# Performance work log

Hardware: AMD Instinct MI355X
Metric: run time of the kernel (lower is better)

Reference implementation:

```python
import jax, jax.numpy as jnp
import numpy as np

H = 128; N = 64; B = 128; L = 3; F = 7; E = 64; LAT = 128
NEG = -1e9

def _ln(x, g, b, eps=1e-5):
    m = jnp.mean(x, axis=-1, keepdims=True)
    v = jnp.mean((x - m) ** 2, axis=-1, keepdims=True)
    return (x - m) / jnp.sqrt(v + eps) * g + b

def setup_inputs() -> dict:
    key = jax.random.key(0)
    ks = iter(jax.random.split(key, 64))
    def w(shape, s=0.05):
        return (jax.random.normal(next(ks), shape, dtype=jnp.float32) * s)
    inp = {}
    inp['battery_features'] = jax.random.normal(next(ks), (B, F), dtype=jnp.float32)
    inp['material_embeddings'] = jax.random.normal(next(ks), (B, N, E), dtype=jnp.float32)
    inp['node_mask'] = (jax.random.uniform(next(ks), (B, N)) > 0.2).astype(jnp.float32)
    # material encoder: Linear(E,H), LN, ReLU, Linear(H,H), LN, ReLU
    inp['enc_W1'] = w((E, H)); inp['enc_b1'] = jnp.zeros((H,))
    inp['enc_g1'] = jnp.ones((H,)); inp['enc_B1'] = jnp.zeros((H,))
    inp['enc_W2'] = w((H, H)); inp['enc_b2'] = jnp.zeros((H,))
    inp['enc_g2'] = jnp.ones((H,)); inp['enc_B2'] = jnp.zeros((H,))
    # per-layer GATv2 params (stacked over L layers)
    inp['Wq'] = w((L, H, H)); inp['bq'] = jnp.zeros((L, H))
    inp['Wk'] = w((L, H, H)); inp['bk'] = jnp.zeros((L, H))
    inp['Wv'] = w((L, H, H)); inp['bv'] = jnp.zeros((L, H))
    inp['We1'] = w((L, 2 * H, H)); inp['be1'] = jnp.zeros((L, H))
    inp['We2'] = w((L, H)); inp['be2'] = jnp.zeros((L,))
    inp['Wo'] = w((L, H, H)); inp['bo'] = jnp.zeros((L, H))
    inp['o_g'] = jnp.ones((L, H)); inp['o_B'] = jnp.zeros((L, H))
    # legacy decoder: Linear(F+H,H), LN, ReLU, Linear(H,LAT), LN, ReLU, Linear(LAT,F)
    inp['dW1'] = w((F + H, H)); inp['db1'] = jnp.zeros((H,))
    inp['dg1'] = jnp.ones((H,)); inp['dB1'] = jnp.zeros((H,))
    inp['dW2'] = w((H, LAT)); inp['db2'] = jnp.zeros((LAT,))
    inp['dg2'] = jnp.ones((LAT,)); inp['dB2'] = jnp.zeros((LAT,))
    inp['dW3'] = w((LAT, F)); inp['db3'] = jnp.zeros((F,))
    return inp

def reference(battery_features, material_embeddings, node_mask,
              enc_W1, enc_b1, enc_g1, enc_B1, enc_W2, enc_b2, enc_g2, enc_B2,
              Wq, bq, Wk, bk, Wv, bv, We1, be1, We2, be2, Wo, bo, o_g, o_B,
              dW1, db1, dg1, dB1, dW2, db2, dg2, dB2, dW3, db3):
    # material encoder (dropout=0 / eval)
    x = material_embeddings  # [B,N,E]
    h = jax.nn.relu(_ln(x @ enc_W1 + enc_b1, enc_g1, enc_B1))
    h = jax.nn.relu(_ln(h @ enc_W2 + enc_b2, enc_g2, enc_B2))
    x = h * node_mask[..., None]  # [B,N,H]
    mask2d = node_mask[:, :, None] * node_mask[:, None, :]  # [B,N,N]
    nlayers = Wq.shape[0]
    for l in range(nlayers):
        q = x @ Wq[l] + bq[l]
        k = x @ Wk[l] + bk[l]
        v = x @ Wv[l] + bv[l]
        # edge MLP on concat(q_i, k_j): split first linear, avoid concat materialization
        hq = q @ We1[l, :H]          # [B,N,H]
        hk = k @ We1[l, H:]          # [B,N,H]
        eh = jax.nn.relu(hq[:, :, None, :] + hk[:, None, :, :] + be1[l])  # [B,N,N,H]
        scores = jnp.einsum('bijh,h->bij', eh, We2[l]) + be2[l]
        scores = jnp.where(mask2d > 0, scores, NEG)
        attn = jax.nn.softmax(scores, axis=-1) * mask2d
        agg = jnp.einsum('bij,bjh->bih', attn, v)
        x = jax.nn.relu(_ln(agg @ Wo[l] + bo[l], o_g[l], o_B[l]))
        x = x * node_mask[..., None]
    # masked mean pooling
    denom = jnp.clip(jnp.sum(node_mask, axis=1, keepdims=True), 1.0, None)
    pooled = jnp.sum(x * node_mask[..., None], axis=1) / denom  # [B,H]
    d = jnp.concatenate([battery_features, pooled], axis=-1)
    z = jax.nn.relu(_ln(d @ dW1 + db1, dg1, dB1))
    z = jax.nn.relu(_ln(z @ dW2 + db2, dg2, dB2))
    return z @ dW3 + db3  # [B,F] predicted properties
```

## Files before the change

kernel.cpp:

```cpp
#include <hip/hip_runtime.h>


constexpr float EPS = 1e-5f;
constexpr float NEGI = -1e9f;

typedef __bf16 bf16x8 __attribute__((ext_vector_type(8)));
typedef float floatx4 __attribute__((ext_vector_type(4)));

__device__ __forceinline__ bf16x8 cvt8(const float* p) {
  float t[8];
  *(float4*)t = *(const float4*)p;
  *(float4*)(t + 4) = *(const float4*)(p + 4);
  bf16x8 r;
#pragma unroll
  for (int j = 0; j < 8; ++j) r[j] = (__bf16)t[j];
  return r;
}

__global__ __launch_bounds__(256) void prep_kernel(
    const float* __restrict__ Wq, const float* __restrict__ bq,
    const float* __restrict__ Wk, const float* __restrict__ bk,
    const float* __restrict__ bv, const float* __restrict__ We1,
    const float* __restrict__ be1,
    const float* __restrict__ eW1, const float* __restrict__ eW2,
    const float* __restrict__ Wv, const float* __restrict__ Wo,
    __bf16* __restrict__ w1pk, __bf16* __restrict__ w2pk,
    __bf16* __restrict__ wcatpk, __bf16* __restrict__ wopk,
    float* __restrict__ bcat) {
  int tid = threadIdx.x, blk = blockIdx.x;
  if (blk < 48) {
    __shared__ float sB[128 * 16];
    __shared__ float sF[128 * 17];
    int jb = blk >> 3, cc = blk & 7;
    int l = jb >> 1, w = jb & 1;
    const float* A = (w ? Wk : Wq) + l * 16384;
    const float* Bm = We1 + l * 32768 + w * 16384;
    int c0 = cc * 16;
    for (int idx = tid; idx < 2048; idx += 256) {
      int m = idx >> 4, c = idx & 15;
      sB[idx] = Bm[m * 128 + c0 + c];
    }
    __syncthreads();
    int r = tid >> 1, c8 = (tid & 1) * 8;
    float acc[8] = {};
    const float4* A4 = (const float4*)(A + r * 128);
#pragma unroll 8
    for (int k4 = 0; k4 < 32; ++k4) {
      float4 a = A4[k4];
      float av[4] = {a.x, a.y, a.z, a.w};
#pragma unroll
      for (int kk = 0; kk < 4; ++kk)
#pragma unroll
        for (int c = 0; c < 8; ++c)
          acc[c] = fmaf(av[kk], sB[(k4 * 4 + kk) * 16 + c8 + c], acc[c]);
    }
    for (int c = 0; c < 8; ++c) sF[r * 17 + c8 + c] = acc[c];
    __syncthreads();
    int kc = tid >> 6, lane = tid & 63;
    int k0 = kc * 32 + (lane >> 4) * 8, n = lane & 15;
    bf16x8 pk;
#pragma unroll
    for (int j = 0; j < 8; ++j) pk[j] = (__bf16)sF[(k0 + j) * 17 + n];
    int ntg = 8 + w * 8 + cc;
    *((bf16x8*)(wcatpk + l * 49152) + (ntg * 4 + kc) * 64 + lane) = pk;
  } else if (blk < 56) {
    int job = blk - 48;
    const float* src;
    __bf16* dst;
    int KCH = 4;
    if (job == 0) { src = eW1; dst = w1pk; KCH = 2; }
    else if (job == 1) { src = eW2; dst = w2pk; }
    else if (job < 5) { int l = job - 2; src = Wv + l * 16384; dst = wcatpk + l * 49152; }
    else { int l = job - 5; src = Wo + l * 16384; dst = wopk + l * 16384; }
    for (int s = tid; s < 8 * KCH * 64; s += 256) {
      int lane = s & 63, q = s >> 6;
      int kc = q % KCH, nt = q / KCH;
      int k0 = kc * 32 + (lane >> 4) * 8, n = nt * 16 + (lane & 15);
      bf16x8 pk;
#pragma unroll
      for (int j = 0; j < 8; ++j) pk[j] = (__bf16)src[(k0 + j) * 128 + n];
      *((bf16x8*)dst + (nt * KCH + kc) * 64 + lane) = pk;
    }
  } else {
    for (int idx = tid; idx < 3 * 384; idx += 256) {
      int l = idx / 384, c = idx % 384;
      float val;
      if (c < 128) {
        val = bv[l * 128 + c];
      } else if (c < 256) {
        int cc = c - 128;
        float s = 0.f;
        for (int k = 0; k < 128; ++k) s += bq[l * 128 + k] * We1[l * 32768 + k * 128 + cc];
        val = s;
      } else {
        int cc = c - 256;
        float s = be1[l * 128 + cc];
        for (int k = 0; k < 128; ++k) s += bk[l * 128 + k] * We1[l * 32768 + 16384 + k * 128 + cc];
        val = s;
      }
      bcat[l * 384 + c] = val;
    }
  }
}

__global__ __launch_bounds__(256) void enc_qkv_kernel(
    const float* __restrict__ emb, const float* __restrict__ mask,
    const float* __restrict__ eb1, const float* __restrict__ eg1, const float* __restrict__ eB1,
    const float* __restrict__ eb2, const float* __restrict__ eg2, const float* __restrict__ eB2,
    const __bf16* __restrict__ w1pk, const __bf16* __restrict__ w2pk,
    const __bf16* __restrict__ wcat0, const float* __restrict__ bcat0,
    float* __restrict__ hq, float* __restrict__ hk, __bf16* __restrict__ vpk) {
  __shared__ float s_T[32 * 132];
  __shared__ __bf16 s_xpk[32 * 128];
  __shared__ float s_m[32], s_r[32];
  int tid = threadIdx.x, lane = tid & 63, wv = tid >> 6;
  int r0 = blockIdx.x * 32;
  int b = blockIdx.x >> 1, kcv = blockIdx.x & 1;
  int cl = lane & 15, quad = lane >> 4;
  int mt = wv & 1, ntb = (wv >> 1) * 4;

  {
    bf16x8 a1[2];
#pragma unroll
    for (int kc = 0; kc < 2; ++kc)
      a1[kc] = cvt8(emb + (r0 + mt * 16 + cl) * 64 + kc * 32 + quad * 8);
    floatx4 acc[4];
#pragma unroll
    for (int n = 0; n < 4; ++n) acc[n] = 0;
#pragma unroll
    for (int kc = 0; kc < 2; ++kc)
#pragma unroll
      for (int n = 0; n < 4; ++n) {
        bf16x8 bfr = *((const bf16x8*)w1pk + ((ntb + n) * 2 + kc) * 64 + lane);
        acc[n] = __builtin_amdgcn_mfma_f32_16x16x32_bf16(a1[kc], bfr, acc[n], 0, 0, 0);
      }
#pragma unroll
    for (int n = 0; n < 4; ++n) {
      int col = (ntb + n) * 16 + cl;
      float bb = eb1[col];
#pragma unroll
      for (int r = 0; r < 4; ++r) s_T[(mt * 16 + quad * 4 + r) * 132 + col] = acc[n][r] + bb;
    }
  }
  __syncthreads();
  {
    int r = tid >> 3, c0 = tid & 7;
    const float* p = s_T + r * 132 + c0;
    float s = 0.f, q = 0.f;
#pragma unroll
    for (int k = 0; k < 16; ++k) { float v = p[k * 8]; s += v; q += v * v; }
    s += __shfl_xor(s, 1); s += __shfl_xor(s, 2); s += __shfl_xor(s, 4);
    q += __shfl_xor(q, 1); q += __shfl_xor(q, 2); q += __shfl_xor(q, 4);
    if (c0 == 0) {
      float m = s * (1.f / 128.f);
      s_m[r] = m;
      s_r[r] = rsqrtf(fmaxf(q * (1.f / 128.f) - m * m, 0.f) + EPS);
    }
  }
  __syncthreads();
  for (int ch = tid; ch < 512; ch += 256) {
    int r = ch >> 4, c8 = (ch & 15) * 8;
    float vals[8];
    *(float4*)vals = *(const float4*)(s_T + r * 132 + c8);
    *(float4*)(vals + 4) = *(const float4*)(s_T + r * 132 + c8 + 4);
    float m = s_m[r], rs = s_r[r];
    bf16x8 pk;
#pragma unroll
    for (int k = 0; k < 8; ++k)
      pk[k] = (__bf16)fmaxf((vals[k] - m) * rs * eg1[c8 + k] + eB1[c8 + k], 0.f);
    *((bf16x8*)s_xpk + ((r >> 4) * 4 + (c8 >> 5)) * 64 + (((c8 >> 3) & 3) * 16 + (r & 15))) = pk;
  }
  __syncthreads();
  {
    floatx4 acc[4];
#pragma unroll
    for (int n = 0; n < 4; ++n) acc[n] = 0;
    bf16x8 a2[4];
#pragma unroll
    for (int kc = 0; kc < 4; ++kc) a2[kc] = *((const bf16x8*)s_xpk + (mt * 4 + kc) * 64 + lane);
#pragma unroll
    for (int kc = 0; kc < 4; ++kc)
#pragma unroll
      for (int n = 0; n < 4; ++n) {
        bf16x8 bfr = *((const bf16x8*)w2pk + ((ntb + n) * 4 + kc) * 64 + lane);
        acc[n] = __builtin_amdgcn_mfma_f32_16x16x32_bf16(a2[kc], bfr, acc[n], 0, 0, 0);
      }
    __syncthreads();
#pragma unroll
    for (int n = 0; n < 4; ++n) {
      int col = (ntb + n) * 16 + cl;
      float bb = eb2[col];
#pragma unroll
      for (int r = 0; r < 4; ++r) s_T[(mt * 16 + quad * 4 + r) * 132 + col] = acc[n][r] + bb;
    }
  }
  __syncthreads();
  {
    int r = tid >> 3, c0 = tid & 7;
    const float* p = s_T + r * 132 + c0;
    float s = 0.f, q = 0.f;
#pragma unroll
    for (int k = 0; k < 16; ++k) { float v = p[k * 8]; s += v; q += v * v; }
    s += __shfl_xor(s, 1); s += __shfl_xor(s, 2); s += __shfl_xor(s, 4);
    q += __shfl_xor(q, 1); q += __shfl_xor(q, 2); q += __shfl_xor(q, 4);
    if (c0 == 0) {
      float m = s * (1.f / 128.f);
      s_m[r] = m;
      s_r[r] = rsqrtf(fmaxf(q * (1.f / 128.f) - m * m, 0.f) + EPS);
    }
  }
  __syncthreads();
  for (int ch = tid; ch < 512; ch += 256) {
    int r = ch >> 4, c8 = (ch & 15) * 8;
    float vals[8];
    *(float4*)vals = *(const float4*)(s_T + r * 132 + c8);
    *(float4*)(vals + 4) = *(const float4*)(s_T + r * 132 + c8 + 4);
    float m = s_m[r], rs = s_r[r], mk = mask[r0 + r];
    bf16x8 pk;
#pragma unroll
    for (int k = 0; k < 8; ++k)
      pk[k] = (__bf16)(fmaxf((vals[k] - m) * rs * eg2[c8 + k] + eB2[c8 + k], 0.f) * mk);
    *((bf16x8*)s_xpk + ((r >> 4) * 4 + (c8 >> 5)) * 64 + (((c8 >> 3) & 3) * 16 + (r & 15))) = pk;
  }
  __syncthreads();
  {
    int ntq = (wv >> 1) * 12;
    bf16x8 aq[4];
#pragma unroll
    for (int kc = 0; kc < 4; ++kc) aq[kc] = *((const bf16x8*)s_xpk + (mt * 4 + kc) * 64 + lane);
    floatx4 acc[12];
#pragma unroll
    for (int n = 0; n < 12; ++n) acc[n] = 0;
#pragma unroll
    for (int kc = 0; kc < 4; ++kc)
#pragma unroll
      for (int n = 0; n < 12; ++n) {
        bf16x8 bfr = *((const bf16x8*)wcat0 + ((ntq + n) * 4 + kc) * 64 + lane);
        acc[n] = __builtin_amdgcn_mfma_f32_16x16x32_bf16(aq[kc], bfr, acc[n], 0, 0, 0);
      }
#pragma unroll
    for (int n = 0; n < 12; ++n) {
      int nt = ntq + n;
      if (nt < 8) {
        int col = nt * 16 + cl;
        float bb = bcat0[col];
#pragma unroll
        for (int r = 0; r < 4; ++r) s_T[(mt * 16 + quad * 4 + r) * 132 + col] = acc[n][r] + bb;
      } else if (nt < 16) {
        int col = (nt - 8) * 16 + cl;
        float bb = bcat0[128 + col];
#pragma unroll
        for (int r = 0; r < 4; ++r) hq[(r0 + mt * 16 + quad * 4 + r) * 128 + col] = acc[n][r] + bb;
      } else {
        int col = (nt - 16) * 16 + cl;
        float bb = bcat0[256 + col];
#pragma unroll
        for (int r = 0; r < 4; ++r) hk[(r0 + mt * 16 + quad * 4 + r) * 128 + col] = acc[n][r] + bb;
      }
    }
  }
  __syncthreads();
  for (int s = tid; s < 512; s += 256) {
    int lane2 = s & 63, nt = s >> 6;
    int q2 = lane2 >> 4, c2 = lane2 & 15;
    bf16x8 pk;
#pragma unroll
    for (int jj = 0; jj < 8; ++jj) pk[jj] = (__bf16)s_T[(q2 * 8 + jj) * 132 + nt * 16 + c2];
    ((bf16x8*)(vpk + b * 8192))[(nt * 2 + kcv) * 64 + lane2] = pk;
  }
}

template <bool LAST>
__global__ __launch_bounds__(256) void layer_kernel(
    const float* __restrict__ hq_in, const float* __restrict__ hk_in,
    const __bf16* __restrict__ vpk_in, const float* __restrict__ mask,
    const float* __restrict__ We2, const float* __restrict__ be2p,
    const __bf16* __restrict__ wopk_l, const float* __restrict__ bo_l,
    const float* __restrict__ og_l, const float* __restrict__ oB_l,
    const __bf16* __restrict__ wcat_n, const float* __restrict__ bcat_n,
    float* __restrict__ hq_out, float* __restrict__ hk_out,
    __bf16* __restrict__ vpk_out, float* __restrict__ xout) {
  __shared__ float s_hk[64 * 132];
  __shared__ float s_hq[16 * 132];
  __shared__ float s_at[16 * 68];
  __shared__ float s_agg[16 * 132];
  __shared__ float s_T[16 * 132];
  __shared__ __bf16 s_xpk[16 * 128];
  __shared__ float s_m[16], s_r[16];
  __shared__ float s_mk[64];
  int tid = threadIdx.x, lane = tid & 63, wv = tid >> 6;
  int b = blockIdx.x >> 2, i0 = (blockIdx.x & 3) * 16;
  int cl = lane & 15, quad = lane >> 4;

  {
    const float4* src = (const float4*)(hk_in + b * 8192);
    for (int idx = tid; idx < 2048; idx += 256) {
      int row = idx >> 5, c4 = (idx & 31) * 4;
      *(float4*)(s_hk + row * 132 + c4) = src[idx];
    }
    const float4* srq = (const float4*)(hq_in + (b * 64 + i0) * 128);
    for (int idx = tid; idx < 512; idx += 256) {
      int row = idx >> 5, c4 = (idx & 31) * 4;
      *(float4*)(s_hq + row * 132 + c4) = srq[idx];
    }
    if (tid < 64) s_mk[tid] = mask[b * 64 + tid];
  }
  __syncthreads();

  {
    int j = lane;
    float mj = s_mk[j];
    float accs[4] = {};
#pragma unroll
    for (int half = 0; half < 2; ++half) {
      float4 hkv[16], w2v[16];
#pragma unroll
      for (int q = 0; q < 16; ++q) hkv[q] = *(const float4*)(s_hk + j * 132 + half * 64 + q * 4);
#pragma unroll
      for (int q = 0; q < 16; ++q) w2v[q] = *(const float4*)(We2 + half * 64 + q * 4);
#pragma unroll
      for (int kk = 0; kk < 4; ++kk) {
        int il = wv * 4 + kk;
        const float4* hq4 = (const float4*)(s_hq + il * 132 + half * 64);
        float a0 = 0.f, a1 = 0.f, a2 = 0.f, a3 = 0.f;
#pragma unroll
        for (int q = 0; q < 16; ++q) {
          float4 h4 = hq4[q], k4 = hkv[q], w4 = w2v[q];
          a0 = fmaf(fmaxf(h4.x + k4.x, 0.f), w4.x, a0);
          a1 = fmaf(fmaxf(h4.y + k4.y, 0.f), w4.y, a1);
          a2 = fmaf(fmaxf(h4.z + k4.z, 0.f), w4.z, a2);
          a3 = fmaf(fmaxf(h4.w + k4.w, 0.f), w4.w, a3);
        }
        accs[kk] += (a0 + a1) + (a2 + a3);
      }
    }
    float be2v = be2p[0];
#pragma unroll
    for (int kk = 0; kk < 4; ++kk) {
      int il = wv * 4 + kk;
      float m2 = s_mk[i0 + il] * mj;
      float sc = (m2 > 0.f) ? accs[kk] + be2v : NEGI;
      float mx = sc;
#pragma unroll
      for (int off = 32; off >= 1; off >>= 1) mx = fmaxf(mx, __shfl_xor(mx, off));
      float p = __expf(sc - mx);
      float sm = p;
#pragma unroll
      for (int off = 32; off >= 1; off >>= 1) sm += __shfl_xor(sm, off);
      s_at[il * 68 + j] = p / sm * m2;
    }
  }
  __syncthreads();

  {
    bf16x8 aat[2];
#pragma unroll
    for (int kc = 0; kc < 2; ++kc) aat[kc] = cvt8(s_at + cl * 68 + kc * 32 + quad * 8);
    const bf16x8* vb = (const bf16x8*)(vpk_in + b * 8192);
    floatx4 acc[2];
    acc[0] = 0; acc[1] = 0;
#pragma unroll
    for (int kc = 0; kc < 2; ++kc)
#pragma unroll
      for (int n = 0; n < 2; ++n) {
        bf16x8 bfr = vb[((2 * wv + n) * 2 + kc) * 64 + lane];
        acc[n] = __builtin_amdgcn_mfma_f32_16x16x32_bf16(aat[kc], bfr, acc[n], 0, 0, 0);
      }
#pragma unroll
    for (int n = 0; n < 2; ++n) {
      int col = (2 * wv + n) * 16 + cl;
#pragma unroll
      for (int r = 0; r < 4; ++r) s_agg[(quad * 4 + r) * 132 + col] = acc[n][r];
    }
  }
  __syncthreads();

  {
    bf16x8 ag[4];
#pragma unroll
    for (int kc = 0; kc < 4; ++kc) ag[kc] = cvt8(s_agg + cl * 132 + kc * 32 + quad * 8);
    floatx4 acc[2];
    acc[0] = 0; acc[1] = 0;
#pragma unroll
    for (int kc = 0; kc < 4; ++kc)
#pragma unroll
      for (int n = 0; n < 2; ++n) {
        bf16x8 bfr = *((const bf16x8*)wopk_l + ((2 * wv + n) * 4 + kc) * 64 + lane);
        acc[n] = __builtin_amdgcn_mfma_f32_16x16x32_bf16(ag[kc], bfr, acc[n], 0, 0, 0);
      }
#pragma unroll
    for (int n = 0; n < 2; ++n) {
      int col = (2 * wv + n) * 16 + cl;
      float bb = bo_l[col];
#pragma unroll
      for (int r = 0; r < 4; ++r) s_T[(quad * 4 + r) * 132 + col] = acc[n][r] + bb;
    }
  }
  __syncthreads();

  {
    int r = tid >> 4, c0 = tid & 15;
    const float* p = s_T + r * 132 + c0;
    float s = 0.f, q = 0.f;
#pragma unroll
    for (int k = 0; k < 8; ++k) { float v = p[k * 16]; s += v; q += v * v; }
    s += __shfl_xor(s, 1); s += __shfl_xor(s, 2); s += __shfl_xor(s, 4); s += __shfl_xor(s, 8);
    q += __shfl_xor(q, 1); q += __shfl_xor(q, 2); q += __shfl_xor(q, 4); q += __shfl_xor(q, 8);
    if (c0 == 0) {
      float m = s * (1.f / 128.f);
      s_m[r] = m;
      s_r[r] = rsqrtf(fmaxf(q * (1.f / 128.f) - m * m, 0.f) + EPS);
    }
  }
  __syncthreads();
  {
    int r = tid >> 4, c8 = (tid & 15) * 8;
    float vals[8];
    *(float4*)vals = *(const float4*)(s_T + r * 132 + c8);
    *(float4*)(vals + 4) = *(const float4*)(s_T + r * 132 + c8 + 4);
    float m = s_m[r], rs = s_r[r], mk = s_mk[i0 + r];
#pragma unroll
    for (int k = 0; k < 8; ++k)
      vals[k] = fmaxf((vals[k] - m) * rs * og_l[c8 + k] + oB_l[c8 + k], 0.f) * mk;
    if (LAST) {
      float* xp = xout + (b * 64 + i0 + r) * 128 + c8;
      *(float4*)xp = *(float4*)vals;
      *(float4*)(xp + 4) = *(float4*)(vals + 4);
    } else {
      bf16x8 pk;
#pragma unroll
      for (int k = 0; k < 8; ++k) pk[k] = (__bf16)vals[k];
      *((bf16x8*)s_xpk + (c8 >> 5) * 64 + (((c8 >> 3) & 3) * 16 + r)) = pk;
    }
  }
  if (!LAST) {
    __syncthreads();
    {
      bf16x8 ax[4];
#pragma unroll
      for (int kc = 0; kc < 4; ++kc) ax[kc] = *((const bf16x8*)s_xpk + kc * 64 + lane);
      floatx4 acc[6];
#pragma unroll
      for (int n = 0; n < 6; ++n) acc[n] = 0;
#pragma unroll
      for (int kc = 0; kc < 4; ++kc)
#pragma unroll
        for (int n = 0; n < 6; ++n) {
          bf16x8 bfr = *((const bf16x8*)wcat_n + ((wv * 6 + n) * 4 + kc) * 64 + lane);
          acc[n] = __builtin_amdgcn_mfma_f32_16x16x32_bf16(ax[kc], bfr, acc[n], 0, 0, 0);
        }
#pragma unroll
      for (int n = 0; n < 6; ++n) {
        int nt = wv * 6 + n;
        if (nt < 8) {
          int col = nt * 16 + cl;
          float bb = bcat_n[col];
#pragma unroll
          for (int r = 0; r < 4; ++r) s_T[(quad * 4 + r) * 132 + col] = acc[n][r] + bb;
        } else if (nt < 16) {
          int col = (nt - 8) * 16 + cl;
          float bb = bcat_n[128 + col];
#pragma unroll
          for (int r = 0; r < 4; ++r) hq_out[(b * 64 + i0 + quad * 4 + r) * 128 + col] = acc[n][r] + bb;
        } else {
          int col = (nt - 16) * 16 + cl;
          float bb = bcat_n[256 + col];
#pragma unroll
          for (int r = 0; r < 4; ++r) hk_out[(b * 64 + i0 + quad * 4 + r) * 128 + col] = acc[n][r] + bb;
        }
      }
    }
    __syncthreads();
    {
      int kcv = i0 >> 5, q0 = (i0 & 31) >> 3;
      int nt = tid >> 5, dq = (tid >> 4) & 1, c2 = tid & 15;
      int qg = q0 + dq;
      bf16x8 pk;
#pragma unroll
      for (int jj = 0; jj < 8; ++jj) pk[jj] = (__bf16)s_T[(dq * 8 + jj) * 132 + nt * 16 + c2];
      ((bf16x8*)(vpk_out + b * 8192))[(nt * 2 + kcv) * 64 + qg * 16 + c2] = pk;
    }
  }
}

__device__ __forceinline__ float ln128(float val, float g, float be, int t, float* red) {
  float s = val, q = val * val;
#pragma unroll
  for (int off = 32; off >= 1; off >>= 1) {
    s += __shfl_xor(s, off);
    q += __shfl_xor(q, off);
  }
  if ((t & 63) == 0) { red[(t >> 6) * 2] = s; red[(t >> 6) * 2 + 1] = q; }
  __syncthreads();
  float S = red[0] + red[2], Q = red[1] + red[3];
  __syncthreads();
  float m = S * (1.f / 128.f);
  float var = Q * (1.f / 128.f) - m * m;
  float r = rsqrtf(fmaxf(var, 0.f) + EPS);
  return (val - m) * r * g + be;
}

__global__ __launch_bounds__(128) void dec_kernel(
    const float* __restrict__ bf, const float* __restrict__ x, const float* __restrict__ mask,
    const float* __restrict__ dW1, const float* __restrict__ db1,
    const float* __restrict__ dg1, const float* __restrict__ dB1,
    const float* __restrict__ dW2, const float* __restrict__ db2,
    const float* __restrict__ dg2, const float* __restrict__ dB2,
    const float* __restrict__ dW3, const float* __restrict__ db3,
    float* __restrict__ out) {
  __shared__ float s_d[136];
  __shared__ float s_z[128];
  __shared__ float red[4];
  __shared__ float s_mk[64];
  int b = blockIdx.x, t = threadIdx.x;
  if (t < 64) s_mk[t] = mask[b * 64 + t];
  __syncthreads();
  float den = 0.f;
#pragma unroll
  for (int i = 0; i < 64; ++i) den += s_mk[i];
  den = fmaxf(den, 1.f);
  float pooled = 0.f;
  const float* xb = x + b * 8192;
  for (int i = 0; i < 64; ++i) pooled += xb[i * 128 + t];
  pooled /= den;
  if (t < 7) s_d[t] = bf[b * 7 + t];
  s_d[7 + t] = pooled;
  __syncthreads();

  float z = db1[t];
  for (int k = 0; k < 135; ++k) z = fmaf(s_d[k], dW1[k * 128 + t], z);
  z = ln128(z, dg1[t], dB1[t], t, red);
  z = fmaxf(z, 0.f);
  s_z[t] = z;
  __syncthreads();

  float z2 = db2[t];
  for (int k = 0; k < 128; ++k) z2 = fmaf(s_z[k], dW2[k * 128 + t], z2);
  z2 = ln128(z2, dg2[t], dB2[t], t, red);
  z2 = fmaxf(z2, 0.f);
  s_z[t] = z2;
  __syncthreads();

  if (t < 7) {
    float o = db3[t];
    for (int k = 0; k < 128; ++k) o = fmaf(s_z[k], dW3[k * 7 + t], o);
    out[b * 7 + t] = o;
  }
}

extern "C" void kernel_launch(void* const* d_in, const int* in_sizes, int n_in,
                              void* d_out, int out_size, void* d_ws, size_t ws_size,
                              hipStream_t stream) {
  const float* bf   = (const float*)d_in[0];
  const float* emb  = (const float*)d_in[1];
  const float* mask = (const float*)d_in[2];
  const float* eW1 = (const float*)d_in[3];
  const float* eb1 = (const float*)d_in[4];
  const float* eg1 = (const float*)d_in[5];
  const float* eB1 = (const float*)d_in[6];
  const float* eW2 = (const float*)d_in[7];
  const float* eb2 = (const float*)d_in[8];
  const float* eg2 = (const float*)d_in[9];
  const float* eB2 = (const float*)d_in[10];
  const float* Wq = (const float*)d_in[11];
  const float* bq = (const float*)d_in[12];
  const float* Wk = (const float*)d_in[13];
  const float* bk = (const float*)d_in[14];
  const float* Wv = (const float*)d_in[15];
  const float* bv = (const float*)d_in[16];
  const float* We1 = (const float*)d_in[17];
  const float* be1 = (const float*)d_in[18];
  const float* We2 = (const float*)d_in[19];
  const float* be2 = (const float*)d_in[20];
  const float* Wo = (const float*)d_in[21];
  const float* bo = (const float*)d_in[22];
  const float* og = (const float*)d_in[23];
  const float* oB = (const float*)d_in[24];
  const float* dW1 = (const float*)d_in[25];
  const float* db1 = (const float*)d_in[26];
  const float* dg1 = (const float*)d_in[27];
  const float* dB1 = (const float*)d_in[28];
  const float* dW2 = (const float*)d_in[29];
  const float* db2 = (const float*)d_in[30];
  const float* dg2 = (const float*)d_in[31];
  const float* dB2 = (const float*)d_in[32];
  const float* dW3 = (const float*)d_in[33];
  const float* db3 = (const float*)d_in[34];
  float* out = (float*)d_out;

  float* ws = (float*)d_ws;
  float* hqA  = ws;
  float* hkA  = ws + 1048576;
  float* hqB  = ws + 2 * 1048576;
  float* hkB  = ws + 3 * 1048576;
  float* x    = ws + 4 * 1048576;
  float* bcat = ws + 5 * 1048576;
  __bf16* bb16  = (__bf16*)(ws + 5 * 1048576 + 2048);
  __bf16* vpkA  = bb16;
  __bf16* vpkB  = bb16 + 1048576;
  __bf16* wcatpk = bb16 + 2 * 1048576;
  __bf16* wopk   = wcatpk + 3 * 49152;
  __bf16* w1pk   = wopk + 3 * 16384;
  __bf16* w2pk   = w1pk + 8192;

  prep_kernel<<<57, 256, 0, stream>>>(Wq, bq, Wk, bk, bv, We1, be1,
                                      eW1, eW2, Wv, Wo, w1pk, w2pk, wcatpk, wopk, bcat);
  enc_qkv_kernel<<<256, 256, 0, stream>>>(emb, mask, eb1, eg1, eB1, eb2, eg2, eB2,
                                          w1pk, w2pk, wcatpk, bcat, hqA, hkA, vpkA);
  layer_kernel<false><<<512, 256, 0, stream>>>(
      hqA, hkA, vpkA, mask, We2, be2, wopk, bo, og, oB,
      wcatpk + 49152, bcat + 384, hqB, hkB, vpkB, nullptr);
  layer_kernel<false><<<512, 256, 0, stream>>>(
      hqB, hkB, vpkB, mask, We2 + 128, be2 + 1, wopk + 16384, bo + 128, og + 128, oB + 128,
      wcatpk + 2 * 49152, bcat + 2 * 384, hqA, hkA, vpkA, nullptr);
  layer_kernel<true><<<512, 256, 0, stream>>>(
      hqA, hkA, vpkA, mask, We2 + 256, be2 + 2, wopk + 2 * 16384, bo + 256, og + 256, oB + 256,
      nullptr, nullptr, nullptr, nullptr, nullptr, x);
  dec_kernel<<<128, 128, 0, stream>>>(bf, x, mask, dW1, db1, dg1, dB1,
                                      dW2, db2, dg2, dB2, dW3, db3, out);
}
```

Baseline: 223.4 us.

## Fuse encoder, all GAT layers and decoder into one per-batch mega kernel

Replaces the encoder, three per-layer kernels and the decoder with a single 512-thread kernel, one block per batch element, that keeps activations, hq/hk and V in shared memory across layers. The edge-score loop now works in packed fp16 pairs with dot2 accumulation, pooling is folded into the last LayerNorm, and the decoder matvecs are split over four thread groups. This removes global round trips and launch gaps between stages. In exchange only 128 blocks run, which leaves much of the GPU idle, and the fp16 edge scores reduce precision.

```diff
diff --git a/kernel.cpp b/kernel.cpp
--- a/kernel.cpp
+++ b/kernel.cpp
@@ -6,6 +6,9 @@
 
 typedef __bf16 bf16x8 __attribute__((ext_vector_type(8)));
 typedef float floatx4 __attribute__((ext_vector_type(4)));
+typedef _Float16 h2 __attribute__((ext_vector_type(2)));
+
+union U32H2 { unsigned int u; h2 h; };
 
 __device__ __forceinline__ bf16x8 cvt8(const float* p) {
   float t[8];
@@ -15,6 +18,14 @@
 #pragma unroll
   for (int j = 0; j < 8; ++j) r[j] = (__bf16)t[j];
   return r;
+}
+
+__device__ __forceinline__ float fdot2h(h2 a, h2 b, float c) {
+#if __has_builtin(__builtin_amdgcn_fdot2)
+  return __builtin_amdgcn_fdot2(a, b, c, false);
+#else
+  return c + (float)a[0] * (float)b[0] + (float)a[1] * (float)b[1];
+#endif
 }
 
 __global__ __launch_bounds__(256) void prep_kernel(
@@ -103,448 +114,404 @@
   }
 }
 
-__global__ __launch_bounds__(256) void enc_qkv_kernel(
+__device__ __forceinline__ void ln512(unsigned char* SM, const float* __restrict__ g,
+                                      const float* __restrict__ be, float mreg,
+                                      bool domask, bool dopack, bool dopool, int tid) {
+  float* SF = (float*)(SM + 16384);
+  int r = tid >> 3, c0 = tid & 7;
+  const float* base = SF + r * 128;
+  float s = 0.f, q = 0.f;
+#pragma unroll
+  for (int k = 0; k < 16; ++k) {
+    float v = base[(c0 + 8 * k + 4 * r) & 127];
+    s += v; q += v * v;
+  }
+  s += __shfl_xor(s, 1); s += __shfl_xor(s, 2); s += __shfl_xor(s, 4);
+  q += __shfl_xor(q, 1); q += __shfl_xor(q, 2); q += __shfl_xor(q, 4);
+  float m = s * (1.f / 128.f);
+  float rs = rsqrtf(fmaxf(q * (1.f / 128.f) - m * m, 0.f) + EPS);
+  float mk = domask ? __shfl(mreg, r) : 1.f;
+  int c8 = c0 * 16;
+  float vals[16];
+#pragma unroll
+  for (int tq = 0; tq < 4; ++tq)
+    *(float4*)(vals + tq * 4) = *(const float4*)(base + ((c8 + 4 * r + 4 * tq) & 127));
+#pragma unroll
+  for (int k2 = 0; k2 < 16; ++k2) {
+    int c = c8 + k2;
+    vals[k2] = fmaxf((vals[k2] - m) * rs * g[c] + be[c], 0.f) * mk;
+  }
+  if (dopack) {
+#pragma unroll
+    for (int hh = 0; hh < 2; ++hh) {
+      int ch = c8 + hh * 8;
+      bf16x8 pk;
+#pragma unroll
+      for (int j2 = 0; j2 < 8; ++j2) pk[j2] = (__bf16)vals[hh * 8 + j2];
+      ((bf16x8*)SM)[((r >> 4) * 4 + (ch >> 5)) * 64 + ((ch >> 3) & 3) * 16 + (r & 15)] = pk;
+    }
+  }
+  if (dopool) {
+    float* SP = (float*)(SM + 49152);
+#pragma unroll
+    for (int k2 = 0; k2 < 16; ++k2) {
+      float v = vals[k2];
+      v += __shfl_xor(v, 8); v += __shfl_xor(v, 16); v += __shfl_xor(v, 32);
+      vals[k2] = v;
+    }
+    int lane = tid & 63, wvv = tid >> 6;
+    if ((lane >> 3) == 0) {
+#pragma unroll
+      for (int tq = 0; tq < 4; ++tq)
+        *(float4*)(SP + wvv * 128 + c8 + tq * 4) = *(float4*)(vals + tq * 4);
+    }
+  }
+}
+
+__global__ __launch_bounds__(512, 2) void mega_kernel(
     const float* __restrict__ emb, const float* __restrict__ mask,
+    const float* __restrict__ bfeat,
     const float* __restrict__ eb1, const float* __restrict__ eg1, const float* __restrict__ eB1,
     const float* __restrict__ eb2, const float* __restrict__ eg2, const float* __restrict__ eB2,
     const __bf16* __restrict__ w1pk, const __bf16* __restrict__ w2pk,
-    const __bf16* __restrict__ wcat0, const float* __restrict__ bcat0,
-    float* __restrict__ hq, float* __restrict__ hk, __bf16* __restrict__ vpk) {
-  __shared__ float s_T[32 * 132];
-  __shared__ __bf16 s_xpk[32 * 128];
-  __shared__ float s_m[32], s_r[32];
-  int tid = threadIdx.x, lane = tid & 63, wv = tid >> 6;
-  int r0 = blockIdx.x * 32;
-  int b = blockIdx.x >> 1, kcv = blockIdx.x & 1;
-  int cl = lane & 15, quad = lane >> 4;
-  int mt = wv & 1, ntb = (wv >> 1) * 4;
-
-  {
-    bf16x8 a1[2];
-#pragma unroll
-    for (int kc = 0; kc < 2; ++kc)
-      a1[kc] = cvt8(emb + (r0 + mt * 16 + cl) * 64 + kc * 32 + quad * 8);
-    floatx4 acc[4];
-#pragma unroll
-    for (int n = 0; n < 4; ++n) acc[n] = 0;
-#pragma unroll
-    for (int kc = 0; kc < 2; ++kc)
-#pragma unroll
-      for (int n = 0; n < 4; ++n) {
-        bf16x8 bfr = *((const bf16x8*)w1pk + ((ntb + n) * 2 + kc) * 64 + lane);
-        acc[n] = __builtin_amdgcn_mfma_f32_16x16x32_bf16(a1[kc], bfr, acc[n], 0, 0, 0);
-      }
-#pragma unroll
-    for (int n = 0; n < 4; ++n) {
-      int col = (ntb + n) * 16 + cl;
-      float bb = eb1[col];
-#pragma unroll
-      for (int r = 0; r < 4; ++r) s_T[(mt * 16 + quad * 4 + r) * 132 + col] = acc[n][r] + bb;
-    }
-  }
-  __syncthreads();
-  {
-    int r = tid >> 3, c0 = tid & 7;
-    const float* p = s_T + r * 132 + c0;
-    float s = 0.f, q = 0.f;
-#pragma unroll
-    for (int k = 0; k < 16; ++k) { float v = p[k * 8]; s += v; q += v * v; }
-    s += __shfl_xor(s, 1); s += __shfl_xor(s, 2); s += __shfl_xor(s, 4);
-    q += __shfl_xor(q, 1); q += __shfl_xor(q, 2); q += __shfl_xor(q, 4);
-    if (c0 == 0) {
-      float m = s * (1.f / 128.f);
-      s_m[r] = m;
-      s_r[r] = rsqrtf(fmaxf(q * (1.f / 128.f) - m * m, 0.f) + EPS);
-    }
-  }
-  __syncthreads();
-  for (int ch = tid; ch < 512; ch += 256) {
-    int r = ch >> 4, c8 = (ch & 15) * 8;
-    float vals[8];
-    *(float4*)vals = *(const float4*)(s_T + r * 132 + c8);
-    *(float4*)(vals + 4) = *(const float4*)(s_T + r * 132 + c8 + 4);
-    float m = s_m[r], rs = s_r[r];
-    bf16x8 pk;
-#pragma unroll
-    for (int k = 0; k < 8; ++k)
-      pk[k] = (__bf16)fmaxf((vals[k] - m) * rs * eg1[c8 + k] + eB1[c8 + k], 0.f);
-    *((bf16x8*)s_xpk + ((r >> 4) * 4 + (c8 >> 5)) * 64 + (((c8 >> 3) & 3) * 16 + (r & 15))) = pk;
-  }
-  __syncthreads();
-  {
-    floatx4 acc[4];
-#pragma unroll
-    for (int n = 0; n < 4; ++n) acc[n] = 0;
-    bf16x8 a2[4];
-#pragma unroll
-    for (int kc = 0; kc < 4; ++kc) a2[kc] = *((const bf16x8*)s_xpk + (mt * 4 + kc) * 64 + lane);
-#pragma unroll
-    for (int kc = 0; kc < 4; ++kc)
-#pragma unroll
-      for (int n = 0; n < 4; ++n) {
-        bf16x8 bfr = *((const bf16x8*)w2pk + ((ntb + n) * 4 + kc) * 64 + lane);
-        acc[n] = __builtin_amdgcn_mfma_f32_16x16x32_bf16(a2[kc], bfr, acc[n], 0, 0, 0);
-      }
-    __syncthreads();
-#pragma unroll
-    for (int n = 0; n < 4; ++n) {
-      int col = (ntb + n) * 16 + cl;
-      float bb = eb2[col];
-#pragma unroll
-      for (int r = 0; r < 4; ++r) s_T[(mt * 16 + quad * 4 + r) * 132 + col] = acc[n][r] + bb;
-    }
-  }
-  __syncthreads();
-  {
-    int r = tid >> 3, c0 = tid & 7;
-    const float* p = s_T + r * 132 + c0;
-    float s = 0.f, q = 0.f;
-#pragma unroll
-    for (int k = 0; k < 16; ++k) { float v = p[k * 8]; s += v; q += v * v; }
-    s += __shfl_xor(s, 1); s += __shfl_xor(s, 2); s += __shfl_xor(s, 4);
-    q += __shfl_xor(q, 1); q += __shfl_xor(q, 2); q += __shfl_xor(q, 4);
-    if (c0 == 0) {
-      float m = s * (1.f / 128.f);
-      s_m[r] = m;
-      s_r[r] = rsqrtf(fmaxf(q * (1.f / 128.f) - m * m, 0.f) + EPS);
-    }
-  }
-  __syncthreads();
-  for (int ch = tid; ch < 512; ch += 256) {
-    int r = ch >> 4, c8 = (ch & 15) * 8;
-    float vals[8];
-    *(float4*)vals = *(const float4*)(s_T + r * 132 + c8);
-    *(float4*)(vals + 4) = *(const float4*)(s_T + r * 132 + c8 + 4);
-    float m = s_m[r], rs = s_r[r], mk = mask[r0 + r];
-    bf16x8 pk;
-#pragma unroll
-    for (int k = 0; k < 8; ++k)
-      pk[k] = (__bf16)(fmaxf((vals[k] - m) * rs * eg2[c8 + k] + eB2[c8 + k], 0.f) * mk);
-    *((bf16x8*)s_xpk + ((r >> 4) * 4 + (c8 >> 5)) * 64 + (((c8 >> 3) & 3) * 16 + (r & 15))) = pk;
-  }
-  __syncthreads();
-  {
-    int ntq = (wv >> 1) * 12;
-    bf16x8 aq[4];
-#pragma unroll
-    for (int kc = 0; kc < 4; ++kc) aq[kc] = *((const bf16x8*)s_xpk + (mt * 4 + kc) * 64 + lane);
-    floatx4 acc[12];
-#pragma unroll
-    for (int n = 0; n < 12; ++n) acc[n] = 0;
-#pragma unroll
-    for (int kc = 0; kc < 4; ++kc)
-#pragma unroll
-      for (int n = 0; n < 12; ++n) {
-        bf16x8 bfr = *((const bf16x8*)wcat0 + ((ntq + n) * 4 + kc) * 64 + lane);
-        acc[n] = __builtin_amdgcn_mfma_f32_16x16x32_bf16(aq[kc], bfr, acc[n], 0, 0, 0);
-      }
-#pragma unroll
-    for (int n = 0; n < 12; ++n) {
-      int nt = ntq + n;
-      if (nt < 8) {
-        int col = nt * 16 + cl;
-        float bb = bcat0[col];
-#pragma unroll
-        for (int r = 0; r < 4; ++r) s_T[(mt * 16 + quad * 4 + r) * 132 + col] = acc[n][r] + bb;
-      } else if (nt < 16) {
-        int col = (nt - 8) * 16 + cl;
-        float bb = bcat0[128 + col];
-#pragma unroll
-        for (int r = 0; r < 4; ++r) hq[(r0 + mt * 16 + quad * 4 + r) * 128 + col] = acc[n][r] + bb;
-      } else {
-        int col = (nt - 16) * 16 + cl;
-        float bb = bcat0[256 + col];
-#pragma unroll
-        for (int r = 0; r < 4; ++r) hk[(r0 + mt * 16 + quad * 4 + r) * 128 + col] = acc[n][r] + bb;
-      }
-    }
-  }
-  __syncthreads();
-  for (int s = tid; s < 512; s += 256) {
-    int lane2 = s & 63, nt = s >> 6;
-    int q2 = lane2 >> 4, c2 = lane2 & 15;
-    bf16x8 pk;
-#pragma unroll
-    for (int jj = 0; jj < 8; ++jj) pk[jj] = (__bf16)s_T[(q2 * 8 + jj) * 132 + nt * 16 + c2];
-    ((bf16x8*)(vpk + b * 8192))[(nt * 2 + kcv) * 64 + lane2] = pk;
-  }
-}
-
-template <bool LAST>
-__global__ __launch_bounds__(256) void layer_kernel(
-    const float* __restrict__ hq_in, const float* __restrict__ hk_in,
-    const __bf16* __restrict__ vpk_in, const float* __restrict__ mask,
-    const float* __restrict__ We2, const float* __restrict__ be2p,
-    const __bf16* __restrict__ wopk_l, const float* __restrict__ bo_l,
-    const float* __restrict__ og_l, const float* __restrict__ oB_l,
-    const __bf16* __restrict__ wcat_n, const float* __restrict__ bcat_n,
-    float* __restrict__ hq_out, float* __restrict__ hk_out,
-    __bf16* __restrict__ vpk_out, float* __restrict__ xout) {
-  __shared__ float s_hk[64 * 132];
-  __shared__ float s_hq[16 * 132];
-  __shared__ float s_at[16 * 68];
-  __shared__ float s_agg[16 * 132];
-  __shared__ float s_T[16 * 132];
-  __shared__ __bf16 s_xpk[16 * 128];
-  __shared__ float s_m[16], s_r[16];
-  __shared__ float s_mk[64];
-  int tid = threadIdx.x, lane = tid & 63, wv = tid >> 6;
-  int b = blockIdx.x >> 2, i0 = (blockIdx.x & 3) * 16;
-  int cl = lane & 15, quad = lane >> 4;
-
-  {
-    const float4* src = (const float4*)(hk_in + b * 8192);
-    for (int idx = tid; idx < 2048; idx += 256) {
-      int row = idx >> 5, c4 = (idx & 31) * 4;
-      *(float4*)(s_hk + row * 132 + c4) = src[idx];
-    }
-    const float4* srq = (const float4*)(hq_in + (b * 64 + i0) * 128);
-    for (int idx = tid; idx < 512; idx += 256) {
-      int row = idx >> 5, c4 = (idx & 31) * 4;
-      *(float4*)(s_hq + row * 132 + c4) = srq[idx];
-    }
-    if (tid < 64) s_mk[tid] = mask[b * 64 + tid];
-  }
-  __syncthreads();
-
-  {
-    int j = lane;
-    float mj = s_mk[j];
-    float accs[4] = {};
-#pragma unroll
-    for (int half = 0; half < 2; ++half) {
-      float4 hkv[16], w2v[16];
-#pragma unroll
-      for (int q = 0; q < 16; ++q) hkv[q] = *(const float4*)(s_hk + j * 132 + half * 64 + q * 4);
-#pragma unroll
-      for (int q = 0; q < 16; ++q) w2v[q] = *(const float4*)(We2 + half * 64 + q * 4);
-#pragma unroll
-      for (int kk = 0; kk < 4; ++kk) {
-        int il = wv * 4 + kk;
-        const float4* hq4 = (const float4*)(s_hq + il * 132 + half * 64);
-        float a0 = 0.f, a1 = 0.f, a2 = 0.f, a3 = 0.f;
-#pragma unroll
-        for (int q = 0; q < 16; ++q) {
-          float4 h4 = hq4[q], k4 = hkv[q], w4 = w2v[q];
-          a0 = fmaf(fmaxf(h4.x + k4.x, 0.f), w4.x, a0);
-          a1 = fmaf(fmaxf(h4.y + k4.y, 0.f), w4.y, a1);
-          a2 = fmaf(fmaxf(h4.z + k4.z, 0.f), w4.z, a2);
-          a3 = fmaf(fmaxf(h4.w + k4.w, 0.f), w4.w, a3);
-        }
-        accs[kk] += (a0 + a1) + (a2 + a3);
-      }
-    }
-    float be2v = be2p[0];
-#pragma unroll
-    for (int kk = 0; kk < 4; ++kk) {
-      int il = wv * 4 + kk;
-      float m2 = s_mk[i0 + il] * mj;
-      float sc = (m2 > 0.f) ? accs[kk] + be2v : NEGI;
-      float mx = sc;
-#pragma unroll
-      for (int off = 32; off >= 1; off >>= 1) mx = fmaxf(mx, __shfl_xor(mx, off));
-      float p = __expf(sc - mx);
-      float sm = p;
-#pragma unroll
-      for (int off = 32; off >= 1; off >>= 1) sm += __shfl_xor(sm, off);
-      s_at[il * 68 + j] = p / sm * m2;
-    }
-  }
-  __syncthreads();
-
-  {
-    bf16x8 aat[2];
-#pragma unroll
-    for (int kc = 0; kc < 2; ++kc) aat[kc] = cvt8(s_at + cl * 68 + kc * 32 + quad * 8);
-    const bf16x8* vb = (const bf16x8*)(vpk_in + b * 8192);
-    floatx4 acc[2];
-    acc[0] = 0; acc[1] = 0;
-#pragma unroll
-    for (int kc = 0; kc < 2; ++kc)
-#pragma unroll
-      for (int n = 0; n < 2; ++n) {
-        bf16x8 bfr = vb[((2 * wv + n) * 2 + kc) * 64 + lane];
-        acc[n] = __builtin_amdgcn_mfma_f32_16x16x32_bf16(aat[kc], bfr, acc[n], 0, 0, 0);
-      }
-#pragma unroll
-    for (int n = 0; n < 2; ++n) {
-      int col = (2 * wv + n) * 16 + cl;
-#pragma unroll
-      for (int r = 0; r < 4; ++r) s_agg[(quad * 4 + r) * 132 + col] = acc[n][r];
-    }
-  }
-  __syncthreads();
-
-  {
-    bf16x8 ag[4];
-#pragma unroll
-    for (int kc = 0; kc < 4; ++kc) ag[kc] = cvt8(s_agg + cl * 132 + kc * 32 + quad * 8);
-    floatx4 acc[2];
-    acc[0] = 0; acc[1] = 0;
-#pragma unroll
-    for (int kc = 0; kc < 4; ++kc)
-#pragma unroll
-      for (int n = 0; n < 2; ++n) {
-        bf16x8 bfr = *((const bf16x8*)wopk_l + ((2 * wv + n) * 4 + kc) * 64 + lane);
-        acc[n] = __builtin_amdgcn_mfma_f32_16x16x32_bf16(ag[kc], bfr, acc[n], 0, 0, 0);
-      }
-#pragma unroll
-    for (int n = 0; n < 2; ++n) {
-      int col = (2 * wv + n) * 16 + cl;
-      float bb = bo_l[col];
-#pragma unroll
-      for (int r = 0; r < 4; ++r) s_T[(quad * 4 + r) * 132 + col] = acc[n][r] + bb;
-    }
-  }
-  __syncthreads();
-
-  {
-    int r = tid >> 4, c0 = tid & 15;
-    const float* p = s_T + r * 132 + c0;
-    float s = 0.f, q = 0.f;
-#pragma unroll
-    for (int k = 0; k < 8; ++k) { float v = p[k * 16]; s += v; q += v * v; }
-    s += __shfl_xor(s, 1); s += __shfl_xor(s, 2); s += __shfl_xor(s, 4); s += __shfl_xor(s, 8);
-    q += __shfl_xor(q, 1); q += __shfl_xor(q, 2); q += __shfl_xor(q, 4); q += __shfl_xor(q, 8);
-    if (c0 == 0) {
-      float m = s * (1.f / 128.f);
-      s_m[r] = m;
-      s_r[r] = rsqrtf(fmaxf(q * (1.f / 128.f) - m * m, 0.f) + EPS);
-    }
-  }
-  __syncthreads();
-  {
-    int r = tid >> 4, c8 = (tid & 15) * 8;
-    float vals[8];
-    *(float4*)vals = *(const float4*)(s_T + r * 132 + c8);
-    *(float4*)(vals + 4) = *(const float4*)(s_T + r * 132 + c8 + 4);
-    float m = s_m[r], rs = s_r[r], mk = s_mk[i0 + r];
-#pragma unroll
-    for (int k = 0; k < 8; ++k)
-      vals[k] = fmaxf((vals[k] - m) * rs * og_l[c8 + k] + oB_l[c8 + k], 0.f) * mk;
-    if (LAST) {
-      float* xp = xout + (b * 64 + i0 + r) * 128 + c8;
-      *(float4*)xp = *(float4*)vals;
-      *(float4*)(xp + 4) = *(float4*)(vals + 4);
-    } else {
-      bf16x8 pk;
-#pragma unroll
-      for (int k = 0; k < 8; ++k) pk[k] = (__bf16)vals[k];
-      *((bf16x8*)s_xpk + (c8 >> 5) * 64 + (((c8 >> 3) & 3) * 16 + r)) = pk;
-    }
-  }
-  if (!LAST) {
-    __syncthreads();
-    {
-      bf16x8 ax[4];
-#pragma unroll
-      for (int kc = 0; kc < 4; ++kc) ax[kc] = *((const bf16x8*)s_xpk + kc * 64 + lane);
-      floatx4 acc[6];
-#pragma unroll
-      for (int n = 0; n < 6; ++n) acc[n] = 0;
-#pragma unroll
-      for (int kc = 0; kc < 4; ++kc)
-#pragma unroll
-        for (int n = 0; n < 6; ++n) {
-          bf16x8 bfr = *((const bf16x8*)wcat_n + ((wv * 6 + n) * 4 + kc) * 64 + lane);
-          acc[n] = __builtin_amdgcn_mfma_f32_16x16x32_bf16(ax[kc], bfr, acc[n], 0, 0, 0);
-        }
-#pragma unroll
-      for (int n = 0; n < 6; ++n) {
-        int nt = wv * 6 + n;
-        if (nt < 8) {
-          int col = nt * 16 + cl;
-          float bb = bcat_n[col];
-#pragma unroll
-          for (int r = 0; r < 4; ++r) s_T[(quad * 4 + r) * 132 + col] = acc[n][r] + bb;
-        } else if (nt < 16) {
-          int col = (nt - 8) * 16 + cl;
-          float bb = bcat_n[128 + col];
-#pragma unroll
-          for (int r = 0; r < 4; ++r) hq_out[(b * 64 + i0 + quad * 4 + r) * 128 + col] = acc[n][r] + bb;
-        } else {
-          int col = (nt - 16) * 16 + cl;
-          float bb = bcat_n[256 + col];
-#pragma unroll
-          for (int r = 0; r < 4; ++r) hk_out[(b * 64 + i0 + quad * 4 + r) * 128 + col] = acc[n][r] + bb;
-        }
-      }
-    }
-    __syncthreads();
-    {
-      int kcv = i0 >> 5, q0 = (i0 & 31) >> 3;
-      int nt = tid >> 5, dq = (tid >> 4) & 1, c2 = tid & 15;
-      int qg = q0 + dq;
-      bf16x8 pk;
-#pragma unroll
-      for (int jj = 0; jj < 8; ++jj) pk[jj] = (__bf16)s_T[(dq * 8 + jj) * 132 + nt * 16 + c2];
-      ((bf16x8*)(vpk_out + b * 8192))[(nt * 2 + kcv) * 64 + qg * 16 + c2] = pk;
-    }
-  }
-}
-
-__device__ __forceinline__ float ln128(float val, float g, float be, int t, float* red) {
-  float s = val, q = val * val;
-#pragma unroll
-  for (int off = 32; off >= 1; off >>= 1) {
-    s += __shfl_xor(s, off);
-    q += __shfl_xor(q, off);
-  }
-  if ((t & 63) == 0) { red[(t >> 6) * 2] = s; red[(t >> 6) * 2 + 1] = q; }
-  __syncthreads();
-  float S = red[0] + red[2], Q = red[1] + red[3];
-  __syncthreads();
-  float m = S * (1.f / 128.f);
-  float var = Q * (1.f / 128.f) - m * m;
-  float r = rsqrtf(fmaxf(var, 0.f) + EPS);
-  return (val - m) * r * g + be;
-}
-
-__global__ __launch_bounds__(128) void dec_kernel(
-    const float* __restrict__ bf, const float* __restrict__ x, const float* __restrict__ mask,
+    const __bf16* __restrict__ wcatpk, const float* __restrict__ bcat,
+    const float* __restrict__ We2, const float* __restrict__ be2,
+    const __bf16* __restrict__ wopk, const float* __restrict__ bo,
+    const float* __restrict__ og, const float* __restrict__ oB,
     const float* __restrict__ dW1, const float* __restrict__ db1,
     const float* __restrict__ dg1, const float* __restrict__ dB1,
     const float* __restrict__ dW2, const float* __restrict__ db2,
     const float* __restrict__ dg2, const float* __restrict__ dB2,
     const float* __restrict__ dW3, const float* __restrict__ db3,
     float* __restrict__ out) {
-  __shared__ float s_d[136];
-  __shared__ float s_z[128];
-  __shared__ float red[4];
-  __shared__ float s_mk[64];
-  int b = blockIdx.x, t = threadIdx.x;
-  if (t < 64) s_mk[t] = mask[b * 64 + t];
-  __syncthreads();
-  float den = 0.f;
-#pragma unroll
-  for (int i = 0; i < 64; ++i) den += s_mk[i];
+  __shared__ __align__(16) unsigned char SM[65536];
+  __bf16* SX = (__bf16*)SM;
+  unsigned int* LQ = (unsigned int*)(SM + 16384);
+  unsigned int* LK = (unsigned int*)(SM + 32768);
+  float* SF = (float*)(SM + 16384);
+  __bf16* SV = (__bf16*)(SM + 49152);
+  float* SP = (float*)(SM + 49152);
+  float* sd  = (float*)(SM + 53248);
+  float* sz  = (float*)(SM + 53824);
+  float* sz2 = (float*)(SM + 54336);
+  float* red = (float*)(SM + 54848);
+
+  int tid = threadIdx.x;
+  int lane = tid & 63, wv = tid >> 6;
+  int quad = lane >> 4, cl = lane & 15;
+  int b = blockIdx.x;
+  const float* embb = emb + b * 4096;
+  float mreg = mask[b * 64 + lane];
+
+  {
+    bf16x8 a[4][2];
+#pragma unroll
+    for (int mt = 0; mt < 4; ++mt)
+#pragma unroll
+      for (int kc = 0; kc < 2; ++kc)
+        a[mt][kc] = cvt8(embb + (mt * 16 + cl) * 64 + kc * 32 + quad * 8);
+    floatx4 acc[4];
+#pragma unroll
+    for (int mt = 0; mt < 4; ++mt) acc[mt] = 0;
+#pragma unroll
+    for (int kc = 0; kc < 2; ++kc) {
+      bf16x8 bw = *((const bf16x8*)w1pk + (wv * 2 + kc) * 64 + lane);
+#pragma unroll
+      for (int mt = 0; mt < 4; ++mt)
+        acc[mt] = __builtin_amdgcn_mfma_f32_16x16x32_bf16(a[mt][kc], bw, acc[mt], 0, 0, 0);
+    }
+    int col = wv * 16 + cl;
+    float bb = eb1[col];
+#pragma unroll
+    for (int mt = 0; mt < 4; ++mt)
+#pragma unroll
+      for (int r = 0; r < 4; ++r) {
+        int row = mt * 16 + quad * 4 + r;
+        SF[row * 128 + ((col + 4 * row) & 127)] = acc[mt][r] + bb;
+      }
+  }
+  __syncthreads();
+  ln512(SM, eg1, eB1, mreg, false, true, false, tid);
+  __syncthreads();
+
+  {
+    bf16x8 a[4][4];
+#pragma unroll
+    for (int mt = 0; mt < 4; ++mt)
+#pragma unroll
+      for (int kc = 0; kc < 4; ++kc)
+        a[mt][kc] = *((const bf16x8*)SX + (mt * 4 + kc) * 64 + lane);
+    floatx4 acc[4];
+#pragma unroll
+    for (int mt = 0; mt < 4; ++mt) acc[mt] = 0;
+#pragma unroll
+    for (int kc = 0; kc < 4; ++kc) {
+      bf16x8 bw = *((const bf16x8*)w2pk + (wv * 4 + kc) * 64 + lane);
+#pragma unroll
+      for (int mt = 0; mt < 4; ++mt)
+        acc[mt] = __builtin_amdgcn_mfma_f32_16x16x32_bf16(a[mt][kc], bw, acc[mt], 0, 0, 0);
+    }
+    __syncthreads();
+    int col = wv * 16 + cl;
+    float bb = eb2[col];
+#pragma unroll
+    for (int mt = 0; mt < 4; ++mt)
+#pragma unroll
+      for (int r = 0; r < 4; ++r) {
+        int row = mt * 16 + quad * 4 + r;
+        SF[row * 128 + ((col + 4 * row) & 127)] = acc[mt][r] + bb;
+      }
+  }
+  __syncthreads();
+  ln512(SM, eg2, eB2, mreg, true, true, false, tid);
+  __syncthreads();
+
+  for (int l = 0; l < 3; ++l) {
+    const bf16x8* wc = (const bf16x8*)(wcatpk + l * 49152);
+    const bf16x8* wo = (const bf16x8*)(wopk + l * 16384);
+    const float* bc = bcat + l * 384;
+    const float* we2l = We2 + l * 128;
+    float be2v = be2[l];
+    const float* bol = bo + l * 128;
+    const float* ogl = og + l * 128;
+    const float* oBl = oB + l * 128;
+
+    {
+      bf16x8 a[4][4];
+#pragma unroll
+      for (int mt = 0; mt < 4; ++mt)
+#pragma unroll
+        for (int kc = 0; kc < 4; ++kc)
+          a[mt][kc] = *((const bf16x8*)SX + (mt * 4 + kc) * 64 + lane);
+      floatx4 acc[3][4];
+#pragma unroll
+      for (int n = 0; n < 3; ++n)
+#pragma unroll
+        for (int mt = 0; mt < 4; ++mt) acc[n][mt] = 0;
+#pragma unroll
+      for (int kc = 0; kc < 4; ++kc)
+#pragma unroll
+        for (int n = 0; n < 3; ++n) {
+          bf16x8 bw = wc[((wv * 3 + n) * 4 + kc) * 64 + lane];
+#pragma unroll
+          for (int mt = 0; mt < 4; ++mt)
+            acc[n][mt] = __builtin_amdgcn_mfma_f32_16x16x32_bf16(a[mt][kc], bw, acc[n][mt], 0, 0, 0);
+        }
+#pragma unroll
+      for (int n = 0; n < 3; ++n) {
+        int g = wv * 3 + n;
+        if (g < 8) {
+          float bb = bc[g * 16 + cl];
+#pragma unroll
+          for (int mt = 0; mt < 4; ++mt)
+#pragma unroll
+            for (int r = 0; r < 4; ++r) {
+              int j = mt * 16 + quad * 4 + r;
+              SV[((g * 2 + (j >> 5)) * 64 + ((j >> 3) & 3) * 16 + cl) * 8 + (j & 7)] =
+                  (__bf16)(acc[n][mt][r] + bb);
+            }
+        } else if (g < 16) {
+          int h = (g - 8) * 16 + cl;
+          float bb = bc[128 + h];
+          int hp = h >> 1;
+#pragma unroll
+          for (int mt = 0; mt < 4; ++mt)
+#pragma unroll
+            for (int r = 0; r < 4; ++r) {
+              int i = mt * 16 + quad * 4 + r;
+              *(_Float16*)(SM + 16384 + (hp * 64 + ((i + hp) & 63)) * 4 + (h & 1) * 2) =
+                  (_Float16)(acc[n][mt][r] + bb);
+            }
+        } else {
+          int h = (g - 16) * 16 + cl;
+          float bb = bc[256 + h];
+          int hp = h >> 1;
+#pragma unroll
+          for (int mt = 0; mt < 4; ++mt)
+#pragma unroll
+            for (int r = 0; r < 4; ++r) {
+              int j = mt * 16 + quad * 4 + r;
+              *(_Float16*)(SM + 32768 + (hp * 64 + ((j + hp) & 63)) * 4 + (h & 1) * 2) =
+                  (_Float16)(acc[n][mt][r] + bb);
+            }
+        }
+      }
+    }
+    __syncthreads();
+
+    {
+      int i0 = wv * 8;
+      unsigned int hq_u[8];
+#pragma unroll
+      for (int ii = 0; ii < 8; ++ii)
+        hq_u[ii] = LQ[lane * 64 + ((i0 + ii + lane) & 63)];
+      U32H2 w2c;
+      w2c.h[0] = (_Float16)we2l[2 * lane];
+      w2c.h[1] = (_Float16)we2l[2 * lane + 1];
+      float acc8[8];
+#pragma unroll
+      for (int ii = 0; ii < 8; ++ii) acc8[ii] = 0.f;
+      h2 hz = {(_Float16)0.0f, (_Float16)0.0f};
+#pragma unroll
+      for (int hp = 0; hp < 64; ++hp) {
+        U32H2 hk; hk.u = LK[hp * 64 + ((lane + hp) & 63)];
+        U32H2 w2h; w2h.u = (unsigned int)__shfl((int)w2c.u, hp);
+#pragma unroll
+        for (int ii = 0; ii < 8; ++ii) {
+          U32H2 hq; hq.u = (unsigned int)__shfl((int)hq_u[ii], hp);
+          h2 s2 = hq.h + hk.h;
+          s2 = __builtin_elementwise_max(s2, hz);
+          acc8[ii] = fdot2h(s2, w2h.h, acc8[ii]);
+        }
+      }
+      float mj = mreg;
+#pragma unroll
+      for (int ii = 0; ii < 8; ++ii) {
+        int i = i0 + ii;
+        float mi = __shfl(mreg, i);
+        float m2 = mi * mj;
+        float sc = (m2 > 0.f) ? acc8[ii] + be2v : NEGI;
+        float mx = sc;
+#pragma unroll
+        for (int off = 32; off >= 1; off >>= 1) mx = fmaxf(mx, __shfl_xor(mx, off));
+        float p = __expf(sc - mx);
+        float sm = p;
+#pragma unroll
+        for (int off = 32; off >= 1; off >>= 1) sm += __shfl_xor(sm, off);
+        ((__bf16*)SM)[i * 72 + lane] = (__bf16)(p / sm * m2);
+      }
+    }
+    __syncthreads();
+
+    {
+      bf16x8 aat[4][2];
+#pragma unroll
+      for (int mt = 0; mt < 4; ++mt)
+#pragma unroll
+        for (int kc = 0; kc < 2; ++kc)
+          aat[mt][kc] = *(const bf16x8*)(SM + ((mt * 16 + cl) * 72 + kc * 32 + quad * 8) * 2);
+      __syncthreads();
+      floatx4 acc[4];
+#pragma unroll
+      for (int mt = 0; mt < 4; ++mt) acc[mt] = 0;
+#pragma unroll
+      for (int kc = 0; kc < 2; ++kc) {
+        bf16x8 bw = ((const bf16x8*)SV)[(wv * 2 + kc) * 64 + lane];
+#pragma unroll
+        for (int mt = 0; mt < 4; ++mt)
+          acc[mt] = __builtin_amdgcn_mfma_f32_16x16x32_bf16(aat[mt][kc], bw, acc[mt], 0, 0, 0);
+      }
+      int hcol = wv * 16 + cl;
+      int kc2 = hcol >> 5, q2 = (hcol >> 3) & 3, jj = hcol & 7;
+#pragma unroll
+      for (int mt = 0; mt < 4; ++mt)
+#pragma unroll
+        for (int r = 0; r < 4; ++r) {
+          int i = mt * 16 + quad * 4 + r;
+          SX[((mt * 4 + kc2) * 64 + q2 * 16 + (i & 15)) * 8 + jj] = (__bf16)acc[mt][r];
+        }
+    }
+    __syncthreads();
+
+    {
+      bf16x8 a[4][4];
+#pragma unroll
+      for (int mt = 0; mt < 4; ++mt)
+#pragma unroll
+        for (int kc = 0; kc < 4; ++kc)
+          a[mt][kc] = *((const bf16x8*)SX + (mt * 4 + kc) * 64 + lane);
+      floatx4 acc[4];
+#pragma unroll
+      for (int mt = 0; mt < 4; ++mt) acc[mt] = 0;
+#pragma unroll
+      for (int kc = 0; kc < 4; ++kc) {
+        bf16x8 bw = wo[(wv * 4 + kc) * 64 + lane];
+#pragma unroll
+        for (int mt = 0; mt < 4; ++mt)
+          acc[mt] = __builtin_amdgcn_mfma_f32_16x16x32_bf16(a[mt][kc], bw, acc[mt], 0, 0, 0);
+      }
+      int col = wv * 16 + cl;
+      float bb = bol[col];
+#pragma unroll
+      for (int mt = 0; mt < 4; ++mt)
+#pragma unroll
+        for (int r = 0; r < 4; ++r) {
+          int row = mt * 16 + quad * 4 + r;
+          SF[row * 128 + ((col + 4 * row) & 127)] = acc[mt][r] + bb;
+        }
+    }
+    __syncthreads();
+    ln512(SM, ogl, oBl, mreg, true, l < 2, l == 2, tid);
+    __syncthreads();
+  }
+
+  float den = mreg;
+#pragma unroll
+  for (int off = 32; off >= 1; off >>= 1) den += __shfl_xor(den, off);
   den = fmaxf(den, 1.f);
-  float pooled = 0.f;
-  const float* xb = x + b * 8192;
-  for (int i = 0; i < 64; ++i) pooled += xb[i * 128 + t];
-  pooled /= den;
-  if (t < 7) s_d[t] = bf[b * 7 + t];
-  s_d[7 + t] = pooled;
-  __syncthreads();
-
-  float z = db1[t];
-  for (int k = 0; k < 135; ++k) z = fmaf(s_d[k], dW1[k * 128 + t], z);
-  z = ln128(z, dg1[t], dB1[t], t, red);
-  z = fmaxf(z, 0.f);
-  s_z[t] = z;
-  __syncthreads();
-
-  float z2 = db2[t];
-  for (int k = 0; k < 128; ++k) z2 = fmaf(s_z[k], dW2[k * 128 + t], z2);
-  z2 = ln128(z2, dg2[t], dB2[t], t, red);
-  z2 = fmaxf(z2, 0.f);
-  s_z[t] = z2;
-  __syncthreads();
-
-  if (t < 7) {
-    float o = db3[t];
-    for (int k = 0; k < 128; ++k) o = fmaf(s_z[k], dW3[k * 7 + t], o);
-    out[b * 7 + t] = o;
+
+  if (tid < 7) sd[tid] = bfeat[b * 7 + tid];
+  if (tid < 128) {
+    float s = 0.f;
+#pragma unroll
+    for (int w = 0; w < 8; ++w) s += SP[w * 128 + tid];
+    sd[7 + tid] = s / den;
+  }
+  __syncthreads();
+
+  int t = tid & 127, g4 = tid >> 7;
+  {
+    float zp = 0.f;
+    for (int k = g4; k < 135; k += 4) zp = fmaf(sd[k], dW1[k * 128 + t], zp);
+    SP[g4 * 128 + t] = zp;
+  }
+  __syncthreads();
+  float z = db1[t] + SP[t] + SP[128 + t] + SP[256 + t] + SP[384 + t];
+  {
+    float s = z, q = z * z;
+#pragma unroll
+    for (int off = 32; off >= 1; off >>= 1) { s += __shfl_xor(s, off); q += __shfl_xor(q, off); }
+    if (lane == 0) { red[wv] = s; red[8 + wv] = q; }
+    __syncthreads();
+    float S = 0.f, Q = 0.f;
+#pragma unroll
+    for (int w = 0; w < 8; ++w) { S += red[w]; Q += red[8 + w]; }
+    S *= 0.25f; Q *= 0.25f;
+    float m = S * (1.f / 128.f);
+    float rs = rsqrtf(fmaxf(Q * (1.f / 128.f) - m * m, 0.f) + EPS);
+    z = fmaxf((z - m) * rs * dg1[t] + dB1[t], 0.f);
+    __syncthreads();
+  }
+  sz[t] = z;
+  __syncthreads();
+  {
+    float zp = 0.f;
+    for (int k = g4; k < 128; k += 4) zp = fmaf(sz[k], dW2[k * 128 + t], zp);
+    SP[g4 * 128 + t] = zp;
+  }
+  __syncthreads();
+  float z2 = db2[t] + SP[t] + SP[128 + t] + SP[256 + t] + SP[384 + t];
+  {
+    float s = z2, q = z2 * z2;
+#pragma unroll
+    for (int off = 32; off >= 1; off >>= 1) { s += __shfl_xor(s, off); q += __shfl_xor(q, off); }
+    if (lane == 0) { red[wv] = s; red[8 + wv] = q; }
+    __syncthreads();
+    float S = 0.f, Q = 0.f;
+#pragma unroll
+    for (int w = 0; w < 8; ++w) { S += red[w]; Q += red[8 + w]; }
+    S *= 0.25f; Q *= 0.25f;
+    float m = S * (1.f / 128.f);
+    float rs = rsqrtf(fmaxf(Q * (1.f / 128.f) - m * m, 0.f) + EPS);
+    z2 = fmaxf((z2 - m) * rs * dg2[t] + dB2[t], 0.f);
+    __syncthreads();
+  }
+  sz2[t] = z2;
+  __syncthreads();
+  if (tid < 7) {
+    float o = db3[tid];
+    for (int k = 0; k < 128; ++k) o = fmaf(sz2[k], dW3[k * 7 + tid], o);
+    out[b * 7 + tid] = o;
   }
 }
 
@@ -589,33 +556,16 @@
   float* out = (float*)d_out;
 
   float* ws = (float*)d_ws;
-  float* hqA  = ws;
-  float* hkA  = ws + 1048576;
-  float* hqB  = ws + 2 * 1048576;
-  float* hkB  = ws + 3 * 1048576;
-  float* x    = ws + 4 * 1048576;
-  float* bcat = ws + 5 * 1048576;
-  __bf16* bb16  = (__bf16*)(ws + 5 * 1048576 + 2048);
-  __bf16* vpkA  = bb16;
-  __bf16* vpkB  = bb16 + 1048576;
-  __bf16* wcatpk = bb16 + 2 * 1048576;
+  float* bcat = ws;
+  __bf16* w1pk   = (__bf16*)(ws + 1280);
+  __bf16* w2pk   = w1pk + 8192;
+  __bf16* wcatpk = w2pk + 16384;
   __bf16* wopk   = wcatpk + 3 * 49152;
-  __bf16* w1pk   = wopk + 3 * 16384;
-  __bf16* w2pk   = w1pk + 8192;
 
   prep_kernel<<<57, 256, 0, stream>>>(Wq, bq, Wk, bk, bv, We1, be1,
                                       eW1, eW2, Wv, Wo, w1pk, w2pk, wcatpk, wopk, bcat);
-  enc_qkv_kernel<<<256, 256, 0, stream>>>(emb, mask, eb1, eg1, eB1, eb2, eg2, eB2,
-                                          w1pk, w2pk, wcatpk, bcat, hqA, hkA, vpkA);
-  layer_kernel<false><<<512, 256, 0, stream>>>(
-      hqA, hkA, vpkA, mask, We2, be2, wopk, bo, og, oB,
-      wcatpk + 49152, bcat + 384, hqB, hkB, vpkB, nullptr);
-  layer_kernel<false><<<512, 256, 0, stream>>>(
-      hqB, hkB, vpkB, mask, We2 + 128, be2 + 1, wopk + 16384, bo + 128, og + 128, oB + 128,
-      wcatpk + 2 * 49152, bcat + 2 * 384, hqA, hkA, vpkA, nullptr);
-  layer_kernel<true><<<512, 256, 0, stream>>>(
-      hqA, hkA, vpkA, mask, We2 + 256, be2 + 2, wopk + 2 * 16384, bo + 256, og + 256, oB + 256,
-      nullptr, nullptr, nullptr, nullptr, nullptr, x);
-  dec_kernel<<<128, 128, 0, stream>>>(bf, x, mask, dW1, db1, dg1, dB1,
-                                      dW2, db2, dg2, dB2, dW3, db3, out);
+  mega_kernel<<<128, 512, 0, stream>>>(
+      emb, mask, bf, eb1, eg1, eB1, eb2, eg2, eB2,
+      w1pk, w2pk, wcatpk, bcat, We2, be2, wopk, bo, og, oB,
+      dW1, db1, dg1, dB1, dW2, db2, dg2, dB2, dW3, db3, out);
 }
```

Result: slower. 288.2 us (+29.0%).
